# Optimization experiments

Measured on AMD Instinct MI355X. Metric: run time of the kernel, lower is better.

## Reference

```python
import jax, jax.numpy as jnp
import numpy as np

LEAKY_SLOPE = 0.2
LN_EPS = 1e-5
SOFTMAX_EPS = 1e-16  # PyG softmax denominator eps


def setup_inputs() -> dict:
    key = jax.random.key(0)
    ks = jax.random.split(key, 8)
    N, E, F, H, C, ED = 100000, 1600000, 64, 8, 8, 16
    s = 1.0 / np.sqrt(F)
    return {
        "x": jax.random.normal(ks[0], (N, F), jnp.float32),
        "edge_index": jax.random.randint(ks[1], (2, E), 0, N, jnp.int32),
        "edge_attr": jax.random.normal(ks[2], (E, ED), jnp.float32),
        "W_l": jax.random.normal(ks[3], (H * C, F), jnp.float32) * s,
        "b_l": jnp.zeros((H * C,), jnp.float32),
        "W_r": jax.random.normal(ks[4], (H * C, F), jnp.float32) * s,
        "b_r": jnp.zeros((H * C,), jnp.float32),
        "W_e": jax.random.normal(ks[5], (H * C, ED), jnp.float32) * (1.0 / np.sqrt(ED)),
        "att": jax.random.normal(ks[6], (1, H, C), jnp.float32) * (1.0 / np.sqrt(C)),
        "bias": jnp.zeros((H * C,), jnp.float32),
        "gamma": jnp.ones((F,), jnp.float32),
        "beta": jnp.zeros((F,), jnp.float32),
    }


def reference(x, edge_index, edge_attr, W_l, b_l, W_r, b_r, W_e, att, bias, gamma, beta):
    N, F = x.shape
    H, C = att.shape[1], att.shape[2]
    src, dst = edge_index[0], edge_index[1]  # PyG: row0=source(j), row1=target(i)

    xl = (x @ W_l.T + b_l).reshape(N, H, C)   # lin_l -> x_j side
    xr = (x @ W_r.T + b_r).reshape(N, H, C)   # lin_r -> x_i side
    e = (edge_attr @ W_e.T).reshape(-1, H, C)  # lin_edge (no bias)

    m = jax.nn.leaky_relu(xl[src] + xr[dst] + e, LEAKY_SLOPE)  # [E,H,C]
    logits = jnp.einsum('ehc,hc->eh', m, att[0])               # [E,H]

    # per-destination segment softmax
    mx = jax.ops.segment_max(logits, dst, num_segments=N)      # [N,H]
    mx = jnp.where(jnp.isfinite(mx), mx, 0.0)                  # nodes w/o in-edges
    ex = jnp.exp(logits - mx[dst])
    denom = jax.ops.segment_sum(ex, dst, num_segments=N)
    alpha = ex / (denom[dst] + SOFTMAX_EPS)                    # [E,H]; dropout is identity in eval

    agg = jax.ops.segment_sum(alpha[:, :, None] * xl[src], dst, num_segments=N)  # [N,H,C]
    out = agg.reshape(N, H * C) + bias

    h = out + x  # residual
    mu = jnp.mean(h, axis=-1, keepdims=True)
    var = jnp.mean((h - mu) ** 2, axis=-1, keepdims=True)
    hn = (h - mu) * jax.lax.rsqrt(var + LN_EPS) * gamma + beta
    return jax.nn.relu(hn)
```

## Files before the change

### kernel.cpp

```cpp
#include <hip/hip_runtime.h>

#define LEAKY 0.2f
#define LN_EPS 1e-5f
#define SM_EPS 1e-16f
#define CAP 64
#define WPAD 68

__global__ __launch_bounds__(256) void k_node_linear(
    const float* __restrict__ x,
    const float* __restrict__ Wl,
    const float* __restrict__ bl,
    const float* __restrict__ Wr,
    const float* __restrict__ br,
    float* __restrict__ xl, float* __restrict__ xr,
    int* __restrict__ deg, int N)
{
    __shared__ __align__(16) float sW[64 * WPAD];

    const int tid = threadIdx.x;

    for (int i = blockIdx.x * 256 + tid; i < N; i += gridDim.x * 256) deg[i] = 0;

    const int side = blockIdx.x & 1;
    const float* __restrict__ W  = side ? Wr : Wl;
    const float* __restrict__ bv = side ? br : bl;
    float* __restrict__ dst      = side ? xr : xl;

    for (int i = tid; i < 4096; i += 256)
        sW[(i >> 6) * WPAD + (i & 63)] = W[i];
    __syncthreads();

    const int lane = tid & 63;
    float4 wq[16];
    #pragma unroll
    for (int q = 0; q < 16; ++q)
        wq[q] = *(const float4*)&sW[lane * WPAD + q * 4];
    const float bb = bv[lane];

    const int stream0 = (blockIdx.x >> 1) * 4 + (tid >> 6);
    const int nstream = (gridDim.x >> 1) * 4;
    for (int n = stream0; n < N; n += nstream) {
        const float4* xrow = (const float4*)(x + (long long)n * 64);
        float a = bb;
        #pragma unroll
        for (int q = 0; q < 16; ++q) {
            const float4 xv = xrow[q];
            const float4 w  = wq[q];
            a = fmaf(xv.x, w.x, fmaf(xv.y, w.y, fmaf(xv.z, w.z, fmaf(xv.w, w.w, a))));
        }
        dst[(long long)n * 64 + lane] = a;
    }
}

__global__ __launch_bounds__(256) void k_bucket(
    const int* __restrict__ ei,
    int* __restrict__ deg,
    int* __restrict__ slot,
    int E)
{
    const int base = (blockIdx.x * 256 + threadIdx.x) * 4;
    if (base >= E) return;
    if (((E & 3) == 0) && base + 3 < E) {
        const int4 d4 = *(const int4*)(ei + E + base);
        const int p0 = atomicAdd(deg + d4.x, 1);
        const int p1 = atomicAdd(deg + d4.y, 1);
        const int p2 = atomicAdd(deg + d4.z, 1);
        const int p3 = atomicAdd(deg + d4.w, 1);
        if (p0 < CAP) slot[(long long)d4.x * CAP + p0] = base;
        if (p1 < CAP) slot[(long long)d4.y * CAP + p1] = base + 1;
        if (p2 < CAP) slot[(long long)d4.z * CAP + p2] = base + 2;
        if (p3 < CAP) slot[(long long)d4.w * CAP + p3] = base + 3;
    } else {
        const int hi = (base + 4 < E) ? base + 4 : E;
        for (int e = base; e < hi; ++e) {
            const int dst = ei[E + e];
            const int pos = atomicAdd(deg + dst, 1);
            if (pos < CAP) slot[(long long)dst * CAP + pos] = e;
        }
    }
}

__global__ __launch_bounds__(256) void k_gather(
    const int* __restrict__ ei,
    const float* __restrict__ ea,
    const float* __restrict__ We,
    const float* __restrict__ att,
    const float* __restrict__ xl, const float* __restrict__ xr,
    const int* __restrict__ deg, const int* __restrict__ slot,
    const float* __restrict__ x,
    const float* __restrict__ bias, const float* __restrict__ gamma,
    const float* __restrict__ beta,
    float* __restrict__ out, int N)
{
    const int lane = threadIdx.x & 63;
    const int wid  = blockIdx.x * 4 + (threadIdx.x >> 6);
    const int nw   = gridDim.x * 4;
    if (wid >= N) return;

    const float4* w4 = (const float4*)(We + lane * 16);
    const float4 w0 = w4[0], w1 = w4[1], w2 = w4[2], w3 = w4[3];
    const float attv = att[lane];

    int n = wid;
    int d = min(deg[n], CAP);
    int veid = 0, vsrc = 0;
    if (lane < d) {
        veid = slot[(long long)n * CAP + lane];
        vsrc = ei[veid];
    }
    float xrv = xr[(long long)n * 64 + lane];

    for (;;) {
        const int next = n + nw;
        const int pn = (next < N) ? next : n;
        const int   degN  = deg[pn];
        const int   slotN = slot[(long long)pn * CAP + lane];
        const float xrvN  = xr[(long long)pn * 64 + lane];

        float acc = 0.f;
        float ns  = 0.f;

        float xlA = 0.f, xlB = 0.f;
        float4 a0, a1, a2, a3, b0, b1, b2, b3;
        a0 = a1 = a2 = a3 = b0 = b1 = b2 = b3 = make_float4(0.f, 0.f, 0.f, 0.f);

#define FETCH(j, XLV, E0, E1, E2, E3) do {                           \
            const int s_ = __shfl(vsrc, (j), 64);                    \
            const int e_ = __shfl(veid, (j), 64);                    \
            XLV = xl[(long long)s_ * 64 + lane];                     \
            const float4* p_ = (const float4*)(ea + (long long)e_ * 16); \
            E0 = p_[0]; E1 = p_[1]; E2 = p_[2]; E3 = p_[3];          \
        } while (0)

        if (d > 0) FETCH(0, xlA, a0, a1, a2, a3);
        if (d > 1) FETCH(1, xlB, b0, b1, b2, b3);

        for (int i = 0; i < d; ++i) {
            const float xlc = xlA;
            const float4 c0 = a0, c1 = a1, c2 = a2, c3 = a3;
            xlA = xlB; a0 = b0; a1 = b1; a2 = b2; a3 = b3;
            if (i + 2 < d) FETCH(i + 2, xlB, b0, b1, b2, b3);

            float ep = c0.x*w0.x + c0.y*w0.y + c0.z*w0.z + c0.w*w0.w
                     + c1.x*w1.x + c1.y*w1.y + c1.z*w1.z + c1.w*w1.w
                     + c2.x*w2.x + c2.y*w2.y + c2.z*w2.z + c2.w*w2.w
                     + c3.x*w3.x + c3.y*w3.y + c3.z*w3.z + c3.w*w3.w;
            float m = xlc + xrv + ep;
            m = (m > 0.f) ? m : LEAKY * m;
            float p = m * attv;
            p += __shfl_xor(p, 1, 64);
            p += __shfl_xor(p, 2, 64);
            p += __shfl_xor(p, 4, 64);
            const float ex = __expf(p);
            ns  += ex;
            acc = fmaf(ex, xlc, acc);
        }
#undef FETCH

        const int dN = min(degN, CAP);
        int veidN = 0, vsrcN = 0;
        if (next < N && lane < dN) {
            veidN = slotN;
            vsrcN = ei[veidN];
        }

        const float a = acc / (ns + SM_EPS);
        const float hv = a + bias[lane] + x[(long long)n * 64 + lane];

        float s = hv;
        #pragma unroll
        for (int off = 32; off; off >>= 1) s += __shfl_xor(s, off, 64);
        const float mu = s * (1.f / 64.f);
        const float dd = hv - mu;
        float v = dd * dd;
        #pragma unroll
        for (int off = 32; off; off >>= 1) v += __shfl_xor(v, off, 64);
        const float var = v * (1.f / 64.f);

        float hn = dd * rsqrtf(var + LN_EPS) * gamma[lane] + beta[lane];
        out[(long long)n * 64 + lane] = (hn > 0.f) ? hn : 0.f;

        if (next >= N) break;
        n = next; d = dN; veid = veidN; vsrc = vsrcN; xrv = xrvN;
    }
}

extern "C" void kernel_launch(void* const* d_in, const int* in_sizes, int n_in,
                              void* d_out, int out_size, void* d_ws, size_t ws_size,
                              hipStream_t stream) {
    (void)n_in; (void)ws_size; (void)out_size;

    const float* x     = (const float*)d_in[0];
    const int*   ei    = (const int*)d_in[1];
    const float* ea    = (const float*)d_in[2];
    const float* Wl    = (const float*)d_in[3];
    const float* bl    = (const float*)d_in[4];
    const float* Wr    = (const float*)d_in[5];
    const float* br    = (const float*)d_in[6];
    const float* We    = (const float*)d_in[7];
    const float* att   = (const float*)d_in[8];
    const float* bias  = (const float*)d_in[9];
    const float* gamma = (const float*)d_in[10];
    const float* beta  = (const float*)d_in[11];

    const int N = in_sizes[0] / 64;
    const int E = in_sizes[1] / 2;

    float* w = (float*)d_ws;
    float* xl  = w;                   w += (size_t)N * 64;
    float* xr  = w;                   w += (size_t)N * 64;
    int* deg   = (int*)w;
    int* slot  = deg + N;

    float* out = (float*)d_out;

    k_node_linear<<<2048, 256, 0, stream>>>(
        x, Wl, bl, Wr, br, xl, xr, deg, N);

    const int t2 = (E + 3) / 4;
    k_bucket<<<(t2 + 255) / 256, 256, 0, stream>>>(ei, deg, slot, E);

    k_gather<<<2048, 256, 0, stream>>>(
        ei, ea, We, att, xl, xr, deg, slot, x, bias, gamma, beta, out, N);
}
```

Before: 748.0 us.

## Restructure gather kernel: one wave per node, deeper prefetch, DPP reductions

The gather kernel drops its grid-stride persistent loop and launches one wavefront per destination node, with the grid sized from N. The edge prefetch pipeline goes from two edges in flight to four, rotated through four register sets. Wave shuffles become readlane broadcasts, and the head and LayerNorm reductions use DPP and ds_swizzle. The aim is more memory-level parallelism and cheaper cross-lane ops. The cost is higher register pressure, plus the loss of the next-node metadata prefetch from the old persistent loop.

```diff
diff --git a/kernel.cpp b/kernel.cpp
--- a/kernel.cpp
+++ b/kernel.cpp
@@ -5,6 +5,12 @@
 #define SM_EPS 1e-16f
 #define CAP 64
 #define WPAD 68
+
+#define DPPADD(P, CTRL) \
+    P += __int_as_float(__builtin_amdgcn_update_dpp( \
+        0, __float_as_int(P), CTRL, 0xF, 0xF, true))
+#define SWZADD16(P) \
+    P += __int_as_float(__builtin_amdgcn_ds_swizzle(__float_as_int(P), 0x401F))
 
 __global__ __launch_bounds__(256) void k_node_linear(
     const float* __restrict__ x,
@@ -93,96 +99,97 @@
     float* __restrict__ out, int N)
 {
     const int lane = threadIdx.x & 63;
-    const int wid  = blockIdx.x * 4 + (threadIdx.x >> 6);
-    const int nw   = gridDim.x * 4;
-    if (wid >= N) return;
+    const int n = blockIdx.x * 4 + (threadIdx.x >> 6);
+    if (n >= N) return;
 
     const float4* w4 = (const float4*)(We + lane * 16);
     const float4 w0 = w4[0], w1 = w4[1], w2 = w4[2], w3 = w4[3];
-    const float attv = att[lane];
-
-    int n = wid;
-    int d = min(deg[n], CAP);
+    const float attv  = att[lane];
+    const float xrv   = xr[(long long)n * 64 + lane];
+    const float biasv = bias[lane];
+    const float gv    = gamma[lane];
+    const float bev   = beta[lane];
+    const float xres  = x[(long long)n * 64 + lane];
+
+    const int d = min(deg[n], CAP);
+
     int veid = 0, vsrc = 0;
     if (lane < d) {
         veid = slot[(long long)n * CAP + lane];
         vsrc = ei[veid];
     }
-    float xrv = xr[(long long)n * 64 + lane];
-
-    for (;;) {
-        const int next = n + nw;
-        const int pn = (next < N) ? next : n;
-        const int   degN  = deg[pn];
-        const int   slotN = slot[(long long)pn * CAP + lane];
-        const float xrvN  = xr[(long long)pn * 64 + lane];
-
-        float acc = 0.f;
-        float ns  = 0.f;
-
-        float xlA = 0.f, xlB = 0.f;
-        float4 a0, a1, a2, a3, b0, b1, b2, b3;
-        a0 = a1 = a2 = a3 = b0 = b1 = b2 = b3 = make_float4(0.f, 0.f, 0.f, 0.f);
+
+    float acc = 0.f;
+    float ns  = 0.f;
+
+    float xlA = 0.f, xlB = 0.f, xlC = 0.f, xlD = 0.f;
+    float4 a0, a1, a2, a3, b0, b1, b2, b3, c0, c1, c2, c3, d0, d1, d2, d3;
 
 #define FETCH(j, XLV, E0, E1, E2, E3) do {                           \
-            const int s_ = __shfl(vsrc, (j), 64);                    \
-            const int e_ = __shfl(veid, (j), 64);                    \
-            XLV = xl[(long long)s_ * 64 + lane];                     \
-            const float4* p_ = (const float4*)(ea + (long long)e_ * 16); \
-            E0 = p_[0]; E1 = p_[1]; E2 = p_[2]; E3 = p_[3];          \
-        } while (0)
-
-        if (d > 0) FETCH(0, xlA, a0, a1, a2, a3);
+        const int s_ = __builtin_amdgcn_readlane(vsrc, (j));         \
+        const int e_ = __builtin_amdgcn_readlane(veid, (j));         \
+        XLV = xl[(long long)s_ * 64 + lane];                         \
+        const float4* p_ = (const float4*)(ea + (long long)e_ * 16); \
+        E0 = p_[0]; E1 = p_[1]; E2 = p_[2]; E3 = p_[3];              \
+    } while (0)
+
+#define COMPUTE(XLV, E0, E1, E2, E3) do {                            \
+        float ep = E0.x*w0.x + E0.y*w0.y + E0.z*w0.z + E0.w*w0.w     \
+                 + E1.x*w1.x + E1.y*w1.y + E1.z*w1.z + E1.w*w1.w     \
+                 + E2.x*w2.x + E2.y*w2.y + E2.z*w2.z + E2.w*w2.w     \
+                 + E3.x*w3.x + E3.y*w3.y + E3.z*w3.z + E3.w*w3.w;    \
+        float m = XLV + xrv + ep;                                    \
+        m = (m > 0.f) ? m : LEAKY * m;                               \
+        float p = m * attv;                                          \
+        DPPADD(p, 0xB1);                     \
+        DPPADD(p, 0x4E);                     \
+        DPPADD(p, 0x141);                    \
+        const float ex = __expf(p);                                  \
+        ns  += ex;                                                   \
+        acc = fmaf(ex, XLV, acc);                                    \
+    } while (0)
+
+    if (d > 0) {
+        FETCH(0, xlA, a0, a1, a2, a3);
         if (d > 1) FETCH(1, xlB, b0, b1, b2, b3);
-
-        for (int i = 0; i < d; ++i) {
-            const float xlc = xlA;
-            const float4 c0 = a0, c1 = a1, c2 = a2, c3 = a3;
-            xlA = xlB; a0 = b0; a1 = b1; a2 = b2; a3 = b3;
-            if (i + 2 < d) FETCH(i + 2, xlB, b0, b1, b2, b3);
-
-            float ep = c0.x*w0.x + c0.y*w0.y + c0.z*w0.z + c0.w*w0.w
-                     + c1.x*w1.x + c1.y*w1.y + c1.z*w1.z + c1.w*w1.w
-                     + c2.x*w2.x + c2.y*w2.y + c2.z*w2.z + c2.w*w2.w
-                     + c3.x*w3.x + c3.y*w3.y + c3.z*w3.z + c3.w*w3.w;
-            float m = xlc + xrv + ep;
-            m = (m > 0.f) ? m : LEAKY * m;
-            float p = m * attv;
-            p += __shfl_xor(p, 1, 64);
-            p += __shfl_xor(p, 2, 64);
-            p += __shfl_xor(p, 4, 64);
-            const float ex = __expf(p);
-            ns  += ex;
-            acc = fmaf(ex, xlc, acc);
+        if (d > 2) FETCH(2, xlC, c0, c1, c2, c3);
+        if (d > 3) FETCH(3, xlD, d0, d1, d2, d3);
+        int i = 0;
+        for (;;) {
+            COMPUTE(xlA, a0, a1, a2, a3);
+            if (++i >= d) break;
+            if (i + 3 < d) FETCH(i + 3, xlA, a0, a1, a2, a3);
+            COMPUTE(xlB, b0, b1, b2, b3);
+            if (++i >= d) break;
+            if (i + 3 < d) FETCH(i + 3, xlB, b0, b1, b2, b3);
+            COMPUTE(xlC, c0, c1, c2, c3);
+            if (++i >= d) break;
+            if (i + 3 < d) FETCH(i + 3, xlC, c0, c1, c2, c3);
+            COMPUTE(xlD, d0, d1, d2, d3);
+            if (++i >= d) break;
+            if (i + 3 < d) FETCH(i + 3, xlD, d0, d1, d2, d3);
         }
+    }
 #undef FETCH
-
-        const int dN = min(degN, CAP);
-        int veidN = 0, vsrcN = 0;
-        if (next < N && lane < dN) {
-            veidN = slotN;
-            vsrcN = ei[veidN];
-        }
-
-        const float a = acc / (ns + SM_EPS);
-        const float hv = a + bias[lane] + x[(long long)n * 64 + lane];
-
-        float s = hv;
-        #pragma unroll
-        for (int off = 32; off; off >>= 1) s += __shfl_xor(s, off, 64);
-        const float mu = s * (1.f / 64.f);
-        const float dd = hv - mu;
-        float v = dd * dd;
-        #pragma unroll
-        for (int off = 32; off; off >>= 1) v += __shfl_xor(v, off, 64);
-        const float var = v * (1.f / 64.f);
-
-        float hn = dd * rsqrtf(var + LN_EPS) * gamma[lane] + beta[lane];
-        out[(long long)n * 64 + lane] = (hn > 0.f) ? hn : 0.f;
-
-        if (next >= N) break;
-        n = next; d = dN; veid = veidN; vsrc = vsrcN; xrv = xrvN;
-    }
+#undef COMPUTE
+
+    const float a = acc / (ns + SM_EPS);
+    const float hv = a + biasv + xres;
+
+    float s = hv;
+    DPPADD(s, 0xB1); DPPADD(s, 0x4E); DPPADD(s, 0x141); DPPADD(s, 0x140);
+    SWZADD16(s);
+    s += __shfl_xor(s, 32, 64);
+    const float mu = s * (1.f / 64.f);
+    const float dd = hv - mu;
+    float v = dd * dd;
+    DPPADD(v, 0xB1); DPPADD(v, 0x4E); DPPADD(v, 0x141); DPPADD(v, 0x140);
+    SWZADD16(v);
+    v += __shfl_xor(v, 32, 64);
+    const float var = v * (1.f / 64.f);
+
+    float hn = dd * rsqrtf(var + LN_EPS) * gv + bev;
+    out[(long long)n * 64 + lane] = (hn > 0.f) ? hn : 0.f;
 }
 
 extern "C" void kernel_launch(void* const* d_in, const int* in_sizes, int n_in,
@@ -220,6 +227,6 @@
     const int t2 = (E + 3) / 4;
     k_bucket<<<(t2 + 255) / 256, 256, 0, stream>>>(ei, deg, slot, E);
 
-    k_gather<<<2048, 256, 0, stream>>>(
+    k_gather<<<(N + 3) / 4, 256, 0, stream>>>(
         ei, ea, We, att, xl, xr, deg, slot, x, bias, gamma, beta, out, N);
 }
```

Result: no change. 752.5 us (+0.6%).
